# Kernel optimization log

Hardware: AMD Instinct MI355X
Metric: run time of the kernel (lower is better)

## Reference

```python
import jax, jax.numpy as jnp
import numpy as np
import math

B, H, S, D = 8, 16, 256, 256  # S == D is required by the module's math

def setup_inputs() -> dict:
    key = jax.random.key(0)
    kq, kk, kv, km = jax.random.split(key, 4)
    q = jax.random.normal(kq, (B, H, S, D), dtype=jnp.float32)
    k = jax.random.normal(kk, (B, H, S, D), dtype=jnp.float32)
    v = jax.random.normal(kv, (B, H, S, D), dtype=jnp.float32)
    u = jax.random.uniform(km, (1, H, S, S), dtype=jnp.float32)
    # additive mask: large negative where 'masked', 0.0 elsewhere
    mask = jnp.where(u > 0.7, jnp.float32(-1000.0), jnp.float32(0.0))
    return {"q": q, "k": k, "v": v, "mask": mask}

def reference(q, k, v, mask):
    scale = 1.0 / math.sqrt(q.shape[-1])
    # qk: [B,H,S,S]
    qk = jnp.einsum('bhsd,bhtd->bhst', q, k) * scale + mask
    # first matmul with v: [B,H,S,D] (D == S)
    attn = jnp.einsum('bhst,bhtd->bhsd', qk, v)
    # masked_fill where additive mask == 0.0 (broadcasts [1,H,S,S] -> [B,H,S,D])
    attn = jnp.where(mask == 0.0, jnp.float32(-1e9), attn)
    attn = jax.nn.softmax(attn.astype(jnp.float32), axis=-1).astype(q.dtype)
    # second matmul with v: [B,H,S,D]
    out = jnp.einsum('bhst,bhtd->bhsd', attn, v)
    return out
```

## Files before the change

kernel.cpp:

```cpp
#include <hip/hip_runtime.h>
#include <math.h>

namespace {
constexpr int S  = 256;
constexpr int NT = 256;
constexpr float SCALE = 0.0625f;
constexpr int KLD = 264;
}

typedef __bf16 bf16x4 __attribute__((ext_vector_type(4)));
typedef __bf16 bf16x8 __attribute__((ext_vector_type(8)));
typedef float  f32x4  __attribute__((ext_vector_type(4)));

#define MFMA(a, b, c) __builtin_amdgcn_mfma_f32_16x16x32_bf16((a), (b), (c), 0, 0, 0)

__global__ __launch_bounds__(NT, 4) void prep_kernel(
    const float* __restrict__ q, const float* __restrict__ k,
    const float* __restrict__ v,
    __bf16* __restrict__ vth, __bf16* __restrict__ vtl, __bf16* __restrict__ vtll,
    __bf16* __restrict__ r_hi, __bf16* __restrict__ r_lo,
    int nbh, int swzq)
{
    __shared__ __align__(16) unsigned char lds_arena[32 * KLD * 2 * 2];

    const int tid  = threadIdx.x;
    const int grp  = blockIdx.x / 5;
    const int role = blockIdx.x % 5;

    if (role < 4) {
        __bf16* kh = (__bf16*)lds_arena;
        __bf16* kl = kh + 32 * KLD;

        const int w = tid >> 6, l = tid & 63, l15 = l & 15, l4 = l >> 4;

        int L = grp * 4 + role;
        if (swzq) {
            const int n = nbh * 32;
            L = (L & 7) * (n >> 3) + (L >> 3);
        }
        const int bh = L >> 5;
        const int s0 = ((L >> 3) & 3) << 6;
        const int t0 = (L & 7) << 5;

        const float* qb = q + ((size_t)bh << 16);
        const float* kb = k + ((size_t)bh << 16);

        {
            const float* ksrc = kb + (size_t)t0 * S;
            #pragma unroll 4
            for (int it = 0; it < 8; ++it) {
                const int idx = it * 1024 + tid * 4;
                const float4 f = *(const float4*)&ksrc[idx];
                const float xs[4] = {f.x, f.y, f.z, f.w};
                bf16x4 hv, lv;
                #pragma unroll
                for (int e = 0; e < 4; ++e) {
                    const __bf16 hi = (__bf16)xs[e];
                    hv[e] = hi; lv[e] = (__bf16)(xs[e] - (float)hi);
                }
                const int row = idx >> 8;
                const int col = idx & 255;
                *(bf16x4*)&kh[row * KLD + col] = hv;
                *(bf16x4*)&kl[row * KLD + col] = lv;
            }
        }

        bf16x8 qh[8], ql[8];
        {
            const float* qr = qb + (size_t)(s0 + 16 * w + l15) * S;
            #pragma unroll
            for (int kc = 0; kc < 8; ++kc) {
                const float4 f0 = *(const float4*)&qr[kc * 32 + l4 * 8];
                const float4 f1 = *(const float4*)&qr[kc * 32 + l4 * 8 + 4];
                const float xs[8] = {f0.x, f0.y, f0.z, f0.w, f1.x, f1.y, f1.z, f1.w};
                bf16x8 hv, lv;
                #pragma unroll
                for (int e = 0; e < 8; ++e) {
                    const float x = xs[e] * SCALE;
                    const __bf16 hi = (__bf16)x;
                    hv[e] = hi; lv[e] = (__bf16)(x - (float)hi);
                }
                qh[kc] = hv; ql[kc] = lv;
            }
        }
        __syncthreads();

        f32x4 acc[2];
        acc[0] = (f32x4){0.f, 0.f, 0.f, 0.f};
        acc[1] = (f32x4){0.f, 0.f, 0.f, 0.f};

        #pragma unroll
        for (int kc = 0; kc < 8; ++kc) {
            #pragma unroll
            for (int j = 0; j < 2; ++j) {
                const int bo = (j * 16 + l15) * KLD + kc * 32 + l4 * 8;
                const bf16x8 khf = *(const bf16x8*)&kh[bo];
                const bf16x8 klf = *(const bf16x8*)&kl[bo];
                acc[j] = MFMA(qh[kc], khf, acc[j]);
                acc[j] = MFMA(qh[kc], klf, acc[j]);
                acc[j] = MFMA(ql[kc], khf, acc[j]);
            }
        }
        __syncthreads();

        __bf16* rb = kh;
        #pragma unroll
        for (int j = 0; j < 2; ++j) {
            #pragma unroll
            for (int rr = 0; rr < 4; ++rr) {
                const float rv = acc[j][rr];
                const __bf16 hi = (__bf16)rv;
                const __bf16 lo = (__bf16)(rv - (float)hi);
                const int elem = ((l4 * 4 + rr) + 16 * (2 * j + (l15 >> 3))) * 8
                               + (l15 & 7);
                rb[w * 1024 + elem]       = hi;
                rb[w * 1024 + 512 + elem] = lo;
            }
        }
        const int sb = (s0 >> 4) + w;
        const int tc = t0 >> 5;
        const size_t hb = (size_t)bh << 16;
        const bf16x8 ph = *(const bf16x8*)&rb[w * 1024 + l * 8];
        const bf16x8 pl = *(const bf16x8*)&rb[w * 1024 + 512 + l * 8];
        *(bf16x8*)&r_hi[hb + (size_t)sb * 4096 + (size_t)tc * 512 + l * 8] = ph;
        *(bf16x8*)&r_lo[hb + (size_t)sb * 4096 + (size_t)tc * 512 + l * 8] = pl;
    } else {
        float (*tile)[257] = (float(*)[257])lds_arena;

        const int vi = grp;
        const int bh = vi >> 3;
        const int tc = vi & 7;

        const float* vb = v + (size_t)bh * S * S + (size_t)tc * 32 * S;
        {
            const int c4 = (tid & 63) * 4;
            const int r  = tid >> 6;
            #pragma unroll
            for (int rr = 0; rr < 8; ++rr) {
                const int row = rr * 4 + r;
                const float4 f = *(const float4*)&vb[(size_t)row * S + c4];
                tile[row][c4 + 0] = f.x; tile[row][c4 + 1] = f.y;
                tile[row][c4 + 2] = f.z; tile[row][c4 + 3] = f.w;
            }
        }
        __syncthreads();

        const size_t obase = (size_t)bh * S * S + (size_t)tc * 8192;
        #pragma unroll
        for (int it = 0; it < 4; ++it) {
            const int id  = it * 256 + tid;
            const int j   = id >> 6;
            const int l4  = (id >> 4) & 3;
            const int l15 = id & 15;
            const int d   = j * 16 + l15;
            const int t0  = l4 * 8;
            bf16x8 hv, lv, llv;
            #pragma unroll
            for (int e = 0; e < 8; ++e) {
                const float x = tile[t0 + e][d];
                const __bf16 hi = (__bf16)x;
                const float  hf = (float)hi;
                const __bf16 lo = (__bf16)(x - hf);
                const float  lf = (float)lo;
                hv[e] = hi; lv[e] = lo; llv[e] = (__bf16)(x - hf - lf);
            }
            const size_t oi = obase + (size_t)id * 8;
            *(bf16x8*)&vth[oi]  = hv;
            *(bf16x8*)&vtl[oi]  = lv;
            *(bf16x8*)&vtll[oi] = llv;
        }
    }
}

#define SRC_OF(sp) ((sp) == 0 ? vth : (sp) == 1 ? vtl : vtll)

#define P2_LOAD(tc)                                                           \
    _Pragma("unroll")                                                         \
    for (int r_ = 0; r_ < 12; ++r_) {                                         \
        const int sp_ = r_ >> 2, qt_ = r_ & 3;                                \
        const __bf16* s_ = SRC_OF(sp_);                                       \
        stg[r_] = *(const bf16x8*)&s_[hb + (size_t)(tc) * 8192 + qt_ * 2048 + tid * 8]; \
    }

#define P2_WRITE()                                                            \
    _Pragma("unroll")                                                         \
    for (int r_ = 0; r_ < 12; ++r_) {                                         \
        const int sp_ = r_ >> 2, qt_ = r_ & 3;                                \
        *(bf16x8*)&arena[sp_ * 8192 + qt_ * 2048 + tid * 8] = stg[r_];        \
    }

#define P3_LOAD(tc)                                                           \
    _Pragma("unroll")                                                         \
    for (int r_ = 0; r_ < 8; ++r_) {                                          \
        const int sp_ = r_ >> 2, qt_ = r_ & 3;                                \
        const __bf16* s_ = SRC_OF(sp_);                                       \
        stg[r_] = *(const bf16x8*)&s_[hb + (size_t)(tc) * 8192 + qt_ * 2048 + tid * 8]; \
    }

#define P3_WRITE()                                                            \
    _Pragma("unroll")                                                         \
    for (int r_ = 0; r_ < 8; ++r_) {                                          \
        const int sp_ = r_ >> 2, qt_ = r_ & 3;                                \
        *(bf16x8*)&arena[16384 + sp_ * 8192 + qt_ * 2048 + tid * 8] = stg[r_];\
    }

__global__ __launch_bounds__(NT, 2) void attn2_kernel(
    const float* __restrict__ mask,
    const __bf16* __restrict__ r_hi, const __bf16* __restrict__ r_lo,
    const __bf16* __restrict__ vth, const __bf16* __restrict__ vtl,
    const __bf16* __restrict__ vtll,
    float* __restrict__ out, int H, int swz)
{
    __shared__ __align__(16) __bf16 arena[32768];

    const int tid = threadIdx.x;
    const int w = tid >> 6, l = tid & 63, l15 = l & 15, l4 = l >> 4;

    int L = blockIdx.x;
    if (swz) L = (blockIdx.x & 7) * ((int)gridDim.x >> 3) + (blockIdx.x >> 3);
    const int bh = L >> 2;
    const int s0 = (L & 3) << 6;
    const int h  = bh % H;

    const size_t hb = (size_t)bh << 16;
    const float* mbase = mask + ((size_t)h << 16);

    const int sb_a = (s0 >> 4) + w;
    const __bf16* rh_p = r_hi + hb + (size_t)sb_a * 4096;
    const __bf16* rl_p = r_lo + hb + (size_t)sb_a * 4096;
    const float*  m_p  = mbase + (size_t)(s0 + 16 * w + l15) * S;

    bf16x8 stg[12];

    f32x4 acc2[16];
    #pragma unroll
    for (int j = 0; j < 16; ++j) acc2[j] = (f32x4){0.f, 0.f, 0.f, 0.f};

    P2_LOAD(0);
    P2_WRITE();
    P2_LOAD(1);
    bf16x8 rhc, rlc; float4 m0c, m1c;
    {
        rhc = *(const bf16x8*)&rh_p[l * 8];
        rlc = *(const bf16x8*)&rl_p[l * 8];
        m0c = *(const float4*)&m_p[l4 * 8];
        m1c = *(const float4*)&m_p[l4 * 8 + 4];
    }
    __syncthreads();

    #pragma unroll
    for (int tc = 0; tc < 8; ++tc) {
        bf16x8 rhn, rln; float4 m0n, m1n;
        if (tc < 7) {
            rhn = *(const bf16x8*)&rh_p[(tc + 1) * 512 + l * 8];
            rln = *(const bf16x8*)&rl_p[(tc + 1) * 512 + l * 8];
            const int ko_ = (tc + 1) * 32 + l4 * 8;
            m0n = *(const float4*)&m_p[ko_];
            m1n = *(const float4*)&m_p[ko_ + 4];
        }
        bf16x8 mf;
        mf[0] = (__bf16)m0c.x; mf[1] = (__bf16)m0c.y;
        mf[2] = (__bf16)m0c.z; mf[3] = (__bf16)m0c.w;
        mf[4] = (__bf16)m1c.x; mf[5] = (__bf16)m1c.y;
        mf[6] = (__bf16)m1c.z; mf[7] = (__bf16)m1c.w;

        __builtin_amdgcn_s_setprio(1);
        #pragma unroll
        for (int j = 0; j < 16; ++j) {
            const int fo = j * 512 + l * 8;
            const bf16x8 vh  = *(const bf16x8*)&arena[fo];
            const bf16x8 vl  = *(const bf16x8*)&arena[8192 + fo];
            const bf16x8 vll = *(const bf16x8*)&arena[16384 + fo];
            acc2[j] = MFMA(mf,  vh,  acc2[j]);
            acc2[j] = MFMA(mf,  vl,  acc2[j]);
            acc2[j] = MFMA(mf,  vll, acc2[j]);
            acc2[j] = MFMA(rhc, vh,  acc2[j]);
            acc2[j] = MFMA(rhc, vl,  acc2[j]);
            acc2[j] = MFMA(rlc, vh,  acc2[j]);
        }
        __builtin_amdgcn_s_setprio(0);
        __syncthreads();
        if (tc < 7) {
            P2_WRITE();
            if (tc < 6) P2_LOAD(tc + 2);
            rhc = rhn; rlc = rln; m0c = m0n; m1c = m1n;
            __syncthreads();
        }
    }

    P3_LOAD(0);

    #pragma unroll
    for (int rr = 0; rr < 4; ++rr) {
        const int srow = 16 * w + l4 * 4 + rr;
        const float* mrow = mbase + (size_t)(s0 + srow) * S;
        float mx = -3.4e38f;
        #pragma unroll
        for (int j = 0; j < 16; ++j) {
            const float mval = mrow[j * 16 + l15];
            const float a = (mval == 0.0f) ? -1e9f : acc2[j][rr];
            acc2[j][rr] = a;
            mx = fmaxf(mx, a);
        }
        #pragma unroll
        for (int off = 1; off < 16; off <<= 1)
            mx = fmaxf(mx, __shfl_xor(mx, off, 64));
        float sm = 0.f;
        #pragma unroll
        for (int j = 0; j < 16; ++j) {
            const float e = __expf(acc2[j][rr] - mx);
            acc2[j][rr] = e;
            sm += e;
        }
        #pragma unroll
        for (int off = 1; off < 16; off <<= 1)
            sm += __shfl_xor(sm, off, 64);
        const float inv = 1.0f / sm;
        #pragma unroll
        for (int j = 0; j < 16; ++j) {
            const int t = j * 16 + l15;
            arena[((srow << 8) + t) ^ ((srow & 7) << 3)] = (__bf16)(acc2[j][rr] * inv);
        }
    }
    P3_WRITE();
    P3_LOAD(1);
    __syncthreads();

    f32x4 acc3[16];
    #pragma unroll
    for (int j = 0; j < 16; ++j) acc3[j] = (f32x4){0.f, 0.f, 0.f, 0.f};

    const int prow = 16 * w + l15;
    #pragma unroll
    for (int tc = 0; tc < 8; ++tc) {
        const int pb = ((prow << 8) + tc * 32 + l4 * 8) ^ ((prow & 7) << 3);
        const bf16x8 pa = *(const bf16x8*)&arena[pb];
        __builtin_amdgcn_s_setprio(1);
        #pragma unroll
        for (int j = 0; j < 16; ++j) {
            const int fo = 16384 + j * 512 + l * 8;
            acc3[j] = MFMA(pa, *(const bf16x8*)&arena[fo], acc3[j]);
            acc3[j] = MFMA(pa, *(const bf16x8*)&arena[8192 + fo], acc3[j]);
        }
        __builtin_amdgcn_s_setprio(0);
        __syncthreads();
        if (tc < 7) {
            P3_WRITE();
            if (tc < 6) P3_LOAD(tc + 2);
            __syncthreads();
        }
    }

    float* ob = out + hb + (size_t)s0 * S;
    #pragma unroll
    for (int j = 0; j < 16; ++j) {
        #pragma unroll
        for (int rr = 0; rr < 4; ++rr)
            ob[(size_t)(16 * w + l4 * 4 + rr) * S + j * 16 + l15] = acc3[j][rr];
    }
}

__global__ __launch_bounds__(NT) void transpose_k_kernel(
    const float* __restrict__ k, float* __restrict__ kt)
{
    __shared__ float tile[64][65];
    const int tileIdx = blockIdx.x & 15;
    const int bh      = blockIdx.x >> 4;
    const int ti = (tileIdx >> 2) * 64;
    const int tj = (tileIdx & 3) * 64;
    const float* kb = k  + (size_t)bh * S * S;
    float*      ktb = kt + (size_t)bh * S * S;
    const int c  = threadIdx.x & 63;
    const int r4 = threadIdx.x >> 6;
    #pragma unroll
    for (int rr = 0; rr < 64; rr += 4)
        tile[rr + r4][c] = kb[(size_t)(ti + rr + r4) * S + tj + c];
    __syncthreads();
    #pragma unroll
    for (int rr = 0; rr < 64; rr += 4)
        ktb[(size_t)(tj + rr + r4) * S + ti + c] = tile[c][rr + r4];
}

template <int RPB>
__global__ __launch_bounds__(NT) void fused_attn_rpb(
    const float* __restrict__ q, const float* __restrict__ kt,
    const float* __restrict__ v, const float* __restrict__ mask,
    float* __restrict__ out, int nbh, int H, int swizzle)
{
    __shared__ float qT[S][RPB];
    __shared__ float sT[S][RPB];
    __shared__ float redbuf[4][RPB];

    const int tid = threadIdx.x;
    constexpr int NRB = S / RPB;
    int bh, rb;
    if (swizzle) {
        const int xcd  = blockIdx.x & 7;
        const int slot = blockIdx.x >> 3;
        const int hpx  = nbh >> 3;
        bh = xcd * hpx + (slot % hpx);
        rb = slot / hpx;
    } else {
        bh = blockIdx.x / NRB;
        rb = blockIdx.x % NRB;
    }
    const int h  = bh % H;
    const int s0 = rb * RPB;

    const float* qb  = q    + (size_t)bh * S * S;
    const float* ktb = kt   + (size_t)bh * S * S;
    const float* vb  = v    + (size_t)bh * S * S;
    const float* mb  = mask + (size_t)h  * S * S + (size_t)s0 * S;
    float*       ob  = out  + (size_t)bh * S * S + (size_t)s0 * S;

    #pragma unroll
    for (int si = 0; si < RPB; ++si)
        qT[tid][si] = qb[(size_t)(s0 + si) * S + tid];
    __syncthreads();

    {
        float acc[RPB];
        #pragma unroll
        for (int si = 0; si < RPB; ++si) acc[si] = 0.f;
        #pragma unroll 4
        for (int i = 0; i < S; ++i) {
            const float kv = ktb[(size_t)i * S + tid];
            #pragma unroll
            for (int si4 = 0; si4 < RPB; si4 += 4) {
                const float4 qa = *reinterpret_cast<const float4*>(&qT[i][si4]);
                acc[si4+0] = fmaf(qa.x, kv, acc[si4+0]);
                acc[si4+1] = fmaf(qa.y, kv, acc[si4+1]);
                acc[si4+2] = fmaf(qa.z, kv, acc[si4+2]);
                acc[si4+3] = fmaf(qa.w, kv, acc[si4+3]);
            }
        }
        #pragma unroll
        for (int si4 = 0; si4 < RPB; si4 += 4) {
            float4 t4;
            t4.x = fmaf(acc[si4+0], SCALE, mb[(size_t)(si4+0)*S + tid]);
            t4.y = fmaf(acc[si4+1], SCALE, mb[(size_t)(si4+1)*S + tid]);
            t4.z = fmaf(acc[si4+2], SCALE, mb[(size_t)(si4+2)*S + tid]);
            t4.w = fmaf(acc[si4+3], SCALE, mb[(size_t)(si4+3)*S + tid]);
            *reinterpret_cast<float4*>(&sT[tid][si4]) = t4;
        }
    }
    __syncthreads();

    float a1[RPB];
    #pragma unroll
    for (int si = 0; si < RPB; ++si) a1[si] = 0.f;
    #pragma unroll 2
    for (int t = 0; t < S; ++t) {
        const float vv = vb[(size_t)t * S + tid];
        #pragma unroll
        for (int si4 = 0; si4 < RPB; si4 += 4) {
            const float4 pa = *reinterpret_cast<const float4*>(&sT[t][si4]);
            a1[si4+0] = fmaf(pa.x, vv, a1[si4+0]);
            a1[si4+1] = fmaf(pa.y, vv, a1[si4+1]);
            a1[si4+2] = fmaf(pa.z, vv, a1[si4+2]);
            a1[si4+3] = fmaf(pa.w, vv, a1[si4+3]);
        }
    }
    #pragma unroll
    for (int si = 0; si < RPB; ++si)
        if (mb[(size_t)si * S + tid] == 0.0f) a1[si] = -1e9f;

    const int lane = tid & 63;
    const int wv   = tid >> 6;
    #pragma unroll
    for (int si = 0; si < RPB; ++si) {
        float m = a1[si];
        #pragma unroll
        for (int off = 32; off > 0; off >>= 1)
            m = fmaxf(m, __shfl_down(m, off, 64));
        if (lane == 0) redbuf[wv][si] = m;
    }
    __syncthreads();
    float e[RPB];
    #pragma unroll
    for (int si = 0; si < RPB; ++si) {
        const float m = fmaxf(fmaxf(redbuf[0][si], redbuf[1][si]),
                              fmaxf(redbuf[2][si], redbuf[3][si]));
        e[si] = __expf(a1[si] - m);
    }
    __syncthreads();
    #pragma unroll
    for (int si = 0; si < RPB; ++si) {
        float sm = e[si];
        #pragma unroll
        for (int off = 32; off > 0; off >>= 1)
            sm += __shfl_down(sm, off, 64);
        if (lane == 0) redbuf[wv][si] = sm;
    }
    __syncthreads();
    #pragma unroll
    for (int si4 = 0; si4 < RPB; si4 += 4) {
        float4 t4;
        #pragma unroll
        for (int jj = 0; jj < 4; ++jj) {
            const int si = si4 + jj;
            const float sm = redbuf[0][si] + redbuf[1][si] +
                             redbuf[2][si] + redbuf[3][si];
            (&t4.x)[jj] = e[si] / sm;
        }
        *reinterpret_cast<float4*>(&sT[tid][si4]) = t4;
    }
    __syncthreads();

    float o[RPB];
    #pragma unroll
    for (int si = 0; si < RPB; ++si) o[si] = 0.f;
    #pragma unroll 2
    for (int t = 0; t < S; ++t) {
        const float vv = vb[(size_t)t * S + tid];
        #pragma unroll
        for (int si4 = 0; si4 < RPB; si4 += 4) {
            const float4 pa = *reinterpret_cast<const float4*>(&sT[t][si4]);
            o[si4+0] = fmaf(pa.x, vv, o[si4+0]);
            o[si4+1] = fmaf(pa.y, vv, o[si4+1]);
            o[si4+2] = fmaf(pa.z, vv, o[si4+2]);
            o[si4+3] = fmaf(pa.w, vv, o[si4+3]);
        }
    }
    #pragma unroll
    for (int si = 0; si < RPB; ++si)
        ob[(size_t)si * S + tid] = o[si];
}

extern "C" void kernel_launch(void* const* d_in, const int* in_sizes, int n_in,
                              void* d_out, int out_size, void* d_ws, size_t ws_size,
                              hipStream_t stream) {
    const float* q    = (const float*)d_in[0];
    const float* k    = (const float*)d_in[1];
    const float* v    = (const float*)d_in[2];
    const float* mask = (const float*)d_in[3];
    float* out = (float*)d_out;

    const int nbh = in_sizes[0] / (S * S);
    const int H   = in_sizes[3] / (S * S);
    const size_t he = (size_t)nbh * S * S;
    const size_t need = he * sizeof(__bf16) * 5;
    const size_t kt_bytes = he * sizeof(float);

    if (ws_size >= need) {
        __bf16* vth  = (__bf16*)d_ws;
        __bf16* vtl  = vth + he;
        __bf16* vtll = vtl + he;
        __bf16* rhi  = vtll + he;
        __bf16* rlo  = rhi + he;
        const int nblk_a = nbh * 4;
        const int swza = (nblk_a % 8 == 0) ? 1 : 0;
        prep_kernel<<<dim3(nbh * 40), NT, 0, stream>>>(
            q, k, v, vth, vtl, vtll, rhi, rlo, nbh, 1);
        attn2_kernel<<<dim3(nblk_a), NT, 0, stream>>>(
            mask, rhi, rlo, vth, vtl, vtll, out, H, swza);
    } else if (ws_size >= kt_bytes) {
        float* kt = (float*)d_ws;
        transpose_k_kernel<<<dim3(nbh * 16), NT, 0, stream>>>(k, kt);
        constexpr int RPB = 16;
        const int grid = nbh * (S / RPB);
        const int swz = (nbh % 8 == 0) ? 1 : 0;
        fused_attn_rpb<RPB><<<dim3(grid), NT, 0, stream>>>(
            q, kt, v, mask, out, nbh, H, swz);
    }
}
```

Baseline: 91.98 us.

## Fuse QK^T computation into attention kernel; prep only splits K and V

The prep kernel no longer computes the QK^T tile products. It only converts K into hi/lo bf16 fragments laid out for MFMA, alongside the existing V split. The attention kernel now loads and splits Q into registers and computes each 64x32 QK tile on the fly with split-bf16 MFMAs, staging the result through LDS. This drops the global round-trip of the r_hi/r_lo score intermediates, shrinks the prep grid, and overlaps QK compute with the existing V pipeline. In exchange the attention kernel does more MFMA work, holds more registers for the Q fragments, and reads K fragments directly from global memory.

```diff
diff --git a/kernel.cpp b/kernel.cpp
--- a/kernel.cpp
+++ b/kernel.cpp
@@ -5,7 +5,6 @@
 constexpr int S  = 256;
 constexpr int NT = 256;
 constexpr float SCALE = 0.0625f;
-constexpr int KLD = 264;
 }
 
 typedef __bf16 bf16x4 __attribute__((ext_vector_type(4)));
@@ -15,123 +14,19 @@
 #define MFMA(a, b, c) __builtin_amdgcn_mfma_f32_16x16x32_bf16((a), (b), (c), 0, 0, 0)
 
 __global__ __launch_bounds__(NT, 4) void prep_kernel(
-    const float* __restrict__ q, const float* __restrict__ k,
-    const float* __restrict__ v,
+    const float* __restrict__ k, const float* __restrict__ v,
     __bf16* __restrict__ vth, __bf16* __restrict__ vtl, __bf16* __restrict__ vtll,
-    __bf16* __restrict__ r_hi, __bf16* __restrict__ r_lo,
-    int nbh, int swzq)
+    __bf16* __restrict__ kth, __bf16* __restrict__ ktl)
 {
-    __shared__ __align__(16) unsigned char lds_arena[32 * KLD * 2 * 2];
-
+    __shared__ float tile[32][257];
     const int tid  = threadIdx.x;
-    const int grp  = blockIdx.x / 5;
-    const int role = blockIdx.x % 5;
-
-    if (role < 4) {
-        __bf16* kh = (__bf16*)lds_arena;
-        __bf16* kl = kh + 32 * KLD;
-
-        const int w = tid >> 6, l = tid & 63, l15 = l & 15, l4 = l >> 4;
-
-        int L = grp * 4 + role;
-        if (swzq) {
-            const int n = nbh * 32;
-            L = (L & 7) * (n >> 3) + (L >> 3);
-        }
-        const int bh = L >> 5;
-        const int s0 = ((L >> 3) & 3) << 6;
-        const int t0 = (L & 7) << 5;
-
-        const float* qb = q + ((size_t)bh << 16);
-        const float* kb = k + ((size_t)bh << 16);
-
-        {
-            const float* ksrc = kb + (size_t)t0 * S;
-            #pragma unroll 4
-            for (int it = 0; it < 8; ++it) {
-                const int idx = it * 1024 + tid * 4;
-                const float4 f = *(const float4*)&ksrc[idx];
-                const float xs[4] = {f.x, f.y, f.z, f.w};
-                bf16x4 hv, lv;
-                #pragma unroll
-                for (int e = 0; e < 4; ++e) {
-                    const __bf16 hi = (__bf16)xs[e];
-                    hv[e] = hi; lv[e] = (__bf16)(xs[e] - (float)hi);
-                }
-                const int row = idx >> 8;
-                const int col = idx & 255;
-                *(bf16x4*)&kh[row * KLD + col] = hv;
-                *(bf16x4*)&kl[row * KLD + col] = lv;
-            }
-        }
-
-        bf16x8 qh[8], ql[8];
-        {
-            const float* qr = qb + (size_t)(s0 + 16 * w + l15) * S;
-            #pragma unroll
-            for (int kc = 0; kc < 8; ++kc) {
-                const float4 f0 = *(const float4*)&qr[kc * 32 + l4 * 8];
-                const float4 f1 = *(const float4*)&qr[kc * 32 + l4 * 8 + 4];
-                const float xs[8] = {f0.x, f0.y, f0.z, f0.w, f1.x, f1.y, f1.z, f1.w};
-                bf16x8 hv, lv;
-                #pragma unroll
-                for (int e = 0; e < 8; ++e) {
-                    const float x = xs[e] * SCALE;
-                    const __bf16 hi = (__bf16)x;
-                    hv[e] = hi; lv[e] = (__bf16)(x - (float)hi);
-                }
-                qh[kc] = hv; ql[kc] = lv;
-            }
-        }
-        __syncthreads();
-
-        f32x4 acc[2];
-        acc[0] = (f32x4){0.f, 0.f, 0.f, 0.f};
-        acc[1] = (f32x4){0.f, 0.f, 0.f, 0.f};
-
-        #pragma unroll
-        for (int kc = 0; kc < 8; ++kc) {
-            #pragma unroll
-            for (int j = 0; j < 2; ++j) {
-                const int bo = (j * 16 + l15) * KLD + kc * 32 + l4 * 8;
-                const bf16x8 khf = *(const bf16x8*)&kh[bo];
-                const bf16x8 klf = *(const bf16x8*)&kl[bo];
-                acc[j] = MFMA(qh[kc], khf, acc[j]);
-                acc[j] = MFMA(qh[kc], klf, acc[j]);
-                acc[j] = MFMA(ql[kc], khf, acc[j]);
-            }
-        }
-        __syncthreads();
-
-        __bf16* rb = kh;
-        #pragma unroll
-        for (int j = 0; j < 2; ++j) {
-            #pragma unroll
-            for (int rr = 0; rr < 4; ++rr) {
-                const float rv = acc[j][rr];
-                const __bf16 hi = (__bf16)rv;
-                const __bf16 lo = (__bf16)(rv - (float)hi);
-                const int elem = ((l4 * 4 + rr) + 16 * (2 * j + (l15 >> 3))) * 8
-                               + (l15 & 7);
-                rb[w * 1024 + elem]       = hi;
-                rb[w * 1024 + 512 + elem] = lo;
-            }
-        }
-        const int sb = (s0 >> 4) + w;
-        const int tc = t0 >> 5;
-        const size_t hb = (size_t)bh << 16;
-        const bf16x8 ph = *(const bf16x8*)&rb[w * 1024 + l * 8];
-        const bf16x8 pl = *(const bf16x8*)&rb[w * 1024 + 512 + l * 8];
-        *(bf16x8*)&r_hi[hb + (size_t)sb * 4096 + (size_t)tc * 512 + l * 8] = ph;
-        *(bf16x8*)&r_lo[hb + (size_t)sb * 4096 + (size_t)tc * 512 + l * 8] = pl;
-    } else {
-        float (*tile)[257] = (float(*)[257])lds_arena;
-
-        const int vi = grp;
-        const int bh = vi >> 3;
-        const int tc = vi & 7;
-
-        const float* vb = v + (size_t)bh * S * S + (size_t)tc * 32 * S;
+    const int role = blockIdx.x & 1;
+    const int gi   = blockIdx.x >> 1;
+    const int bh   = gi >> 3;
+    const int c    = gi & 7;
+
+    if (role == 0) {
+        const float* vb = v + (size_t)bh * S * S + (size_t)c * 32 * S;
         {
             const int c4 = (tid & 63) * 4;
             const int r  = tid >> 6;
@@ -145,7 +40,7 @@
         }
         __syncthreads();
 
-        const size_t obase = (size_t)bh * S * S + (size_t)tc * 8192;
+        const size_t obase = (size_t)bh * S * S + (size_t)c * 8192;
         #pragma unroll
         for (int it = 0; it < 4; ++it) {
             const int id  = it * 256 + tid;
@@ -169,6 +64,42 @@
             *(bf16x8*)&vtl[oi]  = lv;
             *(bf16x8*)&vtll[oi] = llv;
         }
+    } else {
+        const float* kb = k + (size_t)bh * S * S + (size_t)c * 32 * S;
+        {
+            const int c4 = (tid & 63) * 4;
+            const int r  = tid >> 6;
+            #pragma unroll
+            for (int rr = 0; rr < 8; ++rr) {
+                const int row = rr * 4 + r;
+                const float4 f = *(const float4*)&kb[(size_t)row * S + c4];
+                tile[row][c4 + 0] = f.x; tile[row][c4 + 1] = f.y;
+                tile[row][c4 + 2] = f.z; tile[row][c4 + 3] = f.w;
+            }
+        }
+        __syncthreads();
+
+        const size_t obase = (size_t)bh * S * S + (size_t)c * 8192;
+        #pragma unroll
+        for (int it = 0; it < 4; ++it) {
+            const int id   = it * 256 + tid;
+            const int t16  = id >> 6;
+            const int l    = id & 63;
+            const int tjl  = t16 >> 3;
+            const int kc   = t16 & 7;
+            const int tl   = tjl * 16 + (l & 15);
+            const int d0   = kc * 32 + (l >> 4) * 8;
+            bf16x8 hv, lv;
+            #pragma unroll
+            for (int e = 0; e < 8; ++e) {
+                const float x = tile[tl][d0 + e];
+                const __bf16 hi = (__bf16)x;
+                hv[e] = hi; lv[e] = (__bf16)(x - (float)hi);
+            }
+            const size_t oi = obase + (size_t)id * 8;
+            *(bf16x8*)&kth[oi] = hv;
+            *(bf16x8*)&ktl[oi] = lv;
+        }
     }
 }
 
@@ -204,9 +135,9 @@
         *(bf16x8*)&arena[16384 + sp_ * 8192 + qt_ * 2048 + tid * 8] = stg[r_];\
     }
 
-__global__ __launch_bounds__(NT, 2) void attn2_kernel(
-    const float* __restrict__ mask,
-    const __bf16* __restrict__ r_hi, const __bf16* __restrict__ r_lo,
+__global__ __launch_bounds__(NT, 2) void fused_attn_kernel(
+    const float* __restrict__ q, const float* __restrict__ mask,
+    const __bf16* __restrict__ kth, const __bf16* __restrict__ ktl,
     const __bf16* __restrict__ vth, const __bf16* __restrict__ vtl,
     const __bf16* __restrict__ vtll,
     float* __restrict__ out, int H, int swz)
@@ -224,11 +155,26 @@
 
     const size_t hb = (size_t)bh << 16;
     const float* mbase = mask + ((size_t)h << 16);
-
-    const int sb_a = (s0 >> 4) + w;
-    const __bf16* rh_p = r_hi + hb + (size_t)sb_a * 4096;
-    const __bf16* rl_p = r_lo + hb + (size_t)sb_a * 4096;
-    const float*  m_p  = mbase + (size_t)(s0 + 16 * w + l15) * S;
+    const float* m_p   = mbase + (size_t)(s0 + 16 * w + l15) * S;
+
+    bf16x8 qh[8], ql[8];
+    {
+        const float* qr = q + hb + (size_t)(s0 + 16 * w + l15) * S;
+        #pragma unroll
+        for (int kc = 0; kc < 8; ++kc) {
+            const float4 f0 = *(const float4*)&qr[kc * 32 + l4 * 8];
+            const float4 f1 = *(const float4*)&qr[kc * 32 + l4 * 8 + 4];
+            const float xs[8] = {f0.x, f0.y, f0.z, f0.w, f1.x, f1.y, f1.z, f1.w};
+            bf16x8 hv, lv;
+            #pragma unroll
+            for (int e = 0; e < 8; ++e) {
+                const float x = xs[e] * SCALE;
+                const __bf16 hi = (__bf16)x;
+                hv[e] = hi; lv[e] = (__bf16)(x - (float)hi);
+            }
+            qh[kc] = hv; ql[kc] = lv;
+        }
+    }
 
     bf16x8 stg[12];
 
@@ -239,21 +185,49 @@
     P2_LOAD(0);
     P2_WRITE();
     P2_LOAD(1);
-    bf16x8 rhc, rlc; float4 m0c, m1c;
-    {
-        rhc = *(const bf16x8*)&rh_p[l * 8];
-        rlc = *(const bf16x8*)&rl_p[l * 8];
-        m0c = *(const float4*)&m_p[l4 * 8];
-        m1c = *(const float4*)&m_p[l4 * 8 + 4];
-    }
-    __syncthreads();
+    float4 m0c = *(const float4*)&m_p[l4 * 8];
+    float4 m1c = *(const float4*)&m_p[l4 * 8 + 4];
+    __syncthreads();
+
+    __bf16* rbp = &arena[24576 + w * 1024];
 
     #pragma unroll
     for (int tc = 0; tc < 8; ++tc) {
-        bf16x8 rhn, rln; float4 m0n, m1n;
+        f32x4 aq0 = (f32x4){0.f, 0.f, 0.f, 0.f};
+        f32x4 aq1 = (f32x4){0.f, 0.f, 0.f, 0.f};
+        #pragma unroll
+        for (int kc = 0; kc < 8; ++kc) {
+            const size_t b0 = hb + (size_t)((2 * tc) * 8 + kc) * 512 + l * 8;
+            const size_t b1 = hb + (size_t)((2 * tc + 1) * 8 + kc) * 512 + l * 8;
+            const bf16x8 k0h = *(const bf16x8*)&kth[b0];
+            const bf16x8 k0l = *(const bf16x8*)&ktl[b0];
+            const bf16x8 k1h = *(const bf16x8*)&kth[b1];
+            const bf16x8 k1l = *(const bf16x8*)&ktl[b1];
+            aq0 = MFMA(qh[kc], k0h, aq0);
+            aq0 = MFMA(qh[kc], k0l, aq0);
+            aq0 = MFMA(ql[kc], k0h, aq0);
+            aq1 = MFMA(qh[kc], k1h, aq1);
+            aq1 = MFMA(qh[kc], k1l, aq1);
+            aq1 = MFMA(ql[kc], k1h, aq1);
+        }
+        #pragma unroll
+        for (int j = 0; j < 2; ++j) {
+            #pragma unroll
+            for (int rr = 0; rr < 4; ++rr) {
+                const float rv = (j ? aq1 : aq0)[rr];
+                const __bf16 hi = (__bf16)rv;
+                const __bf16 lo = (__bf16)(rv - (float)hi);
+                const int elem = ((l4 * 4 + rr) + 16 * (2 * j + (l15 >> 3))) * 8
+                               + (l15 & 7);
+                rbp[elem]       = hi;
+                rbp[512 + elem] = lo;
+            }
+        }
+        const bf16x8 rhc = *(const bf16x8*)&rbp[l * 8];
+        const bf16x8 rlc = *(const bf16x8*)&rbp[512 + l * 8];
+
+        float4 m0n, m1n;
         if (tc < 7) {
-            rhn = *(const bf16x8*)&rh_p[(tc + 1) * 512 + l * 8];
-            rln = *(const bf16x8*)&rl_p[(tc + 1) * 512 + l * 8];
             const int ko_ = (tc + 1) * 32 + l4 * 8;
             m0n = *(const float4*)&m_p[ko_];
             m1n = *(const float4*)&m_p[ko_ + 4];
@@ -283,7 +257,7 @@
         if (tc < 7) {
             P2_WRITE();
             if (tc < 6) P2_LOAD(tc + 2);
-            rhc = rhn; rlc = rln; m0c = m0n; m1c = m1n;
+            m0c = m0n; m1c = m1n;
             __syncthreads();
         }
     }
@@ -546,14 +520,14 @@
         __bf16* vth  = (__bf16*)d_ws;
         __bf16* vtl  = vth + he;
         __bf16* vtll = vtl + he;
-        __bf16* rhi  = vtll + he;
-        __bf16* rlo  = rhi + he;
+        __bf16* kth  = vtll + he;
+        __bf16* ktl  = kth + he;
         const int nblk_a = nbh * 4;
         const int swza = (nblk_a % 8 == 0) ? 1 : 0;
-        prep_kernel<<<dim3(nbh * 40), NT, 0, stream>>>(
-            q, k, v, vth, vtl, vtll, rhi, rlo, nbh, 1);
-        attn2_kernel<<<dim3(nblk_a), NT, 0, stream>>>(
-            mask, rhi, rlo, vth, vtl, vtll, out, H, swza);
+        prep_kernel<<<dim3(nbh * 16), NT, 0, stream>>>(
+            k, v, vth, vtl, vtll, kth, ktl);
+        fused_attn_kernel<<<dim3(nblk_a), NT, 0, stream>>>(
+            q, mask, kth, ktl, vth, vtl, vtll, out, H, swza);
     } else if (ws_size >= kt_bytes) {
         float* kt = (float*)d_ws;
         transpose_k_kernel<<<dim3(nbh * 16), NT, 0, stream>>>(k, kt);
```

New measurement: 110.1 us. +19.7%, slower.
